# Optimization experiments

Hardware: AMD Instinct MI355X
Metric: run time of the kernel (lower is better)

The kernel has to match this reference:

```python
import jax, jax.numpy as jnp
import numpy as np

RES = (64, 64, 64)      # sim.res
INV_DX = 64.0           # sim.inv_dx (n_grid = 64)
P_MASS = 1.0            # sim.p_mass
N = 4_000_000           # n_particles


def setup_inputs() -> dict:
    key = jax.random.key(0)
    k1, k2 = jax.random.split(key)
    # positions in [0.05, 0.95)^3 so the 3x3x3 B-spline stencil stays in-grid
    x = jax.random.uniform(k1, (N, 3), jnp.float32) * 0.9 + 0.05
    x_ref = jax.random.uniform(k2, (N, 3), jnp.float32) * 0.9 + 0.05
    return {"x": x, "x_ref": x_ref}


def _density(x):
    # x: [N, 3] particle positions in [0, 1)
    xs = x * INV_DX
    base = jnp.floor(xs - 0.5).astype(jnp.int32)  # [N, 3]; positions > 0 so floor == trunc (.int() in torch)
    fx = xs - base.astype(x.dtype)                # [N, 3]
    # quadratic B-spline weights, stacked -> [3, N, 3]
    w = jnp.stack([0.5 * (1.5 - fx) ** 2,
                   0.75 - (fx - 1.0) ** 2,
                   0.5 * (fx - 0.5) ** 2])
    density = jnp.zeros(RES, x.dtype)
    # scatter-add over the 27 stencil offsets (equivalent to the unique/mask dedup sum)
    for i in range(3):
        for j in range(3):
            for k in range(3):
                weight = w[i, :, 0] * w[j, :, 1] * w[k, :, 2]  # [N]
                idx = base + jnp.array([i, j, k], jnp.int32)   # [N, 3]
                density = density.at[idx[:, 0], idx[:, 1], idx[:, 2]].add(weight * P_MASS)
    return density


def reference(x, x_ref):
    density = _density(x)
    density_ref = _density(x_ref)
    return jnp.abs(density - density_ref).sum()
```

## Files before the change

kernel.cpp:

```cpp
#include <hip/hip_runtime.h>

#define NRES 64
#define GRID_CELLS (NRES * NRES * NRES)
#define TILE_CELLS 16384
#define TPB 1024
#define QI 2
#define FILL_QUADS (TPB * QI)
#define ZBINS 64
#define NSLABS2 32
#define GC 8
#define CAP 150016u
#define MAXC 32
#define FXS 4194304.0f
#define INV_FXS (1.0f / 4194304.0f)
#define QS 2097152.0f
typedef unsigned long long u64;
typedef unsigned u32;
typedef unsigned short u16;


__device__ __forceinline__ u32 quantc(float v) {
    return (u32)(v * QS + 0.5f);
}
__device__ __forceinline__ int cell_from_q(u32 q) {
    float s = (float)q * (1.0f / 32768.0f);
    int c = (int)(s - 0.5f);
    return min(max(c, 0), 63);
}

__global__ __launch_bounds__(TPB)
void fused_fill_kernel(const float* __restrict__ x, const float* __restrict__ xr,
                       int n, u32* __restrict__ cursor, u64* __restrict__ bins) {
    __shared__ u64 stage[FILL_QUADS * 4];
    __shared__ u32 h[ZBINS];
    __shared__ u32 lb[ZBINS];
    __shared__ u32 gb[ZBINS];
    const int tid = threadIdx.x;
    if (tid < ZBINS) h[tid] = 0;
    __syncthreads();

    const int Q = n >> 2;
    const int GQ = 2 * Q;
    const int g0 = blockIdx.x * FILL_QUADS + tid;

    u64 ent[QI][4];
    u32 lsl[QI][4];
    bool val[QI];

#pragma unroll
    for (int it = 0; it < QI; ++it) {
        int g = g0 + it * TPB;
        val[it] = (g < GQ);
        if (val[it]) {
            int inx = (g < Q);
            const float* __restrict__ p = inx ? (x + 12 * (size_t)g)
                                              : (xr + 12 * (size_t)(g - Q));
            float4 a = ((const float4*)p)[0];
            float4 b = ((const float4*)p)[1];
            float4 c = ((const float4*)p)[2];
            u64 sgn = inx ? 0ull : (1ull << 63);
            float px[4] = {a.x, a.w, b.z, c.y};
            float py[4] = {a.y, b.x, b.w, c.z};
            float pz[4] = {a.z, b.y, c.x, c.w};
#pragma unroll
            for (int q = 0; q < 4; ++q) {
                u32 xq = quantc(px[q]);
                u32 yq = quantc(py[q]);
                u32 zq = quantc(pz[q]);
                ent[it][q] = (u64)xq | ((u64)yq << 21) | ((u64)zq << 42) | sgn;
                int bz = cell_from_q(zq);
                lsl[it][q] = atomicAdd(&h[bz], 1u);
            }
        }
    }
    __syncthreads();

    if (tid < 64) {
        u32 c = h[tid];
        u32 acc = c;
#pragma unroll
        for (int off = 1; off < 64; off <<= 1) {
            u32 o = __shfl_up(acc, off, 64);
            if (tid >= off) acc += o;
        }
        lb[tid] = acc - c;
        gb[tid] = c ? atomicAdd(&cursor[tid], c) : 0u;
    }
    __syncthreads();

#pragma unroll
    for (int it = 0; it < QI; ++it) {
        if (val[it]) {
#pragma unroll
            for (int q = 0; q < 4; ++q) {
                u64 v = ent[it][q];
                int bz = cell_from_q((u32)((v >> 42) & 0x1FFFFFu));
                stage[lb[bz] + lsl[it][q]] = v;
            }
        }
    }
    __syncthreads();

    const int wid = tid >> 6, lane = tid & 63;
    for (int b = wid; b < ZBINS; b += TPB / 64) {
        u32 cnt = h[b];
        u32 l0 = lb[b];
        u32 g  = gb[b];
        u64* __restrict__ dst = bins + (size_t)b * CAP;
        for (u32 i = lane; i < cnt; i += 64) {
            u32 slot = g + i;
            if (slot < CAP) dst[slot] = stage[l0 + i];
        }
    }
}

__global__ __launch_bounds__(TPB)
void bin_scatter_kernel(const u64* __restrict__ bins,
                        const u32* __restrict__ cursor,
                        int* __restrict__ partial) {
    __shared__ int tile[TILE_CELLS];
    const int slab  = blockIdx.x / GC;
    const int chunk = blockIdx.x - slab * GC;

    for (int i = threadIdx.x; i < TILE_CELLS / 4; i += TPB)
        reinterpret_cast<int4*>(tile)[i] = make_int4(0, 0, 0, 0);
    __syncthreads();

    const u32 b0 = (u32)(2 * slab), b1 = b0 + 1;
    u32 c0 = cursor[b0]; if (c0 > CAP) c0 = CAP;
    u32 c1 = cursor[b1]; if (c1 > CAP) c1 = CAP;
    u32 cnt = c0 + c1;
    u32 per = (cnt + (u32)GC - 1u) / (u32)GC;
    u32 i0 = (u32)chunk * per;
    u32 i1 = i0 + per;
    if (i1 > cnt) i1 = cnt;

    for (u32 i = i0 + threadIdx.x; i < i1; i += TPB) {
        u32 idx = (i < c0) ? (b0 * CAP + i) : (b1 * CAP + (i - c0));
        u64 v = bins[idx];
        float xs = (float)(u32)(v & 0x1FFFFFu) * (1.0f / 32768.0f);
        float ys = (float)(u32)((v >> 21) & 0x1FFFFFu) * (1.0f / 32768.0f);
        float zs = (float)(u32)((v >> 42) & 0x1FFFFFu) * (1.0f / 32768.0f);
        float fsgn = (v >> 63) ? -FXS : FXS;

        int bx = (int)(xs - 0.5f);
        int by = (int)(ys - 0.5f);
        int bz = (int)(zs - 0.5f);
        float fx = xs - (float)bx, fy = ys - (float)by, fz = zs - (float)bz;

        float wx0 = 0.5f * (1.5f - fx) * (1.5f - fx);
        float wx1 = 0.75f - (fx - 1.0f) * (fx - 1.0f);
        float wx2 = 0.5f * (fx - 0.5f) * (fx - 0.5f);
        float wy0 = 0.5f * (1.5f - fy) * (1.5f - fy);
        float wy1 = 0.75f - (fy - 1.0f) * (fy - 1.0f);
        float wy2 = 0.5f * (fy - 0.5f) * (fy - 0.5f);
        float wzv[3];
        wzv[0] = 0.5f * (1.5f - fz) * (1.5f - fz);
        wzv[1] = 0.75f - (fz - 1.0f) * (fz - 1.0f);
        wzv[2] = 0.5f * (fz - 0.5f) * (fz - 0.5f);

        float wxy[9];
        wxy[0] = wx0 * wy0; wxy[1] = wx0 * wy1; wxy[2] = wx0 * wy2;
        wxy[3] = wx1 * wy0; wxy[4] = wx1 * wy1; wxy[5] = wx1 * wy2;
        wxy[6] = wx2 * wy0; wxy[7] = wx2 * wy1; wxy[8] = wx2 * wy2;

        int basexy = bx * 64 + by;
        int zlo = bz - 2 * slab;
#pragma unroll
        for (int k = 0; k < 3; ++k) {
            float wzS = wzv[k] * fsgn;
            int a = (zlo + k) * 4096 + basexy;
#pragma unroll
            for (int i2 = 0; i2 < 3; ++i2)
#pragma unroll
                for (int j2 = 0; j2 < 3; ++j2)
                    atomicAdd(&tile[a + i2 * 64 + j2],
                              __float2int_rn(wxy[i2 * 3 + j2] * wzS));
        }
    }
    __syncthreads();

    int* __restrict__ dst = partial + (size_t)blockIdx.x * TILE_CELLS;
    for (int i = threadIdx.x; i < TILE_CELLS / 4; i += TPB)
        reinterpret_cast<int4*>(dst)[i] = reinterpret_cast<const int4*>(tile)[i];
}

__global__ void int_reduce_kernel(const int* __restrict__ partial,
                                  float* __restrict__ out) {
    int tid = blockIdx.x * blockDim.x + threadIdx.x;
    int z  = tid >> 12;
    int xy = tid & 4095;
    int s0 = z >> 1, zl0 = z & 1;
    int sum = 0;
    const int* __restrict__ p0 =
        partial + (size_t)(s0 * GC) * TILE_CELLS + zl0 * 4096 + xy;
#pragma unroll
    for (int g = 0; g < GC; ++g) sum += p0[(size_t)g * TILE_CELLS];
    if (s0 > 0) {
        const int* __restrict__ p1 =
            partial + (size_t)((s0 - 1) * GC) * TILE_CELLS + (zl0 + 2) * 4096 + xy;
#pragma unroll
        for (int g = 0; g < GC; ++g) sum += p1[(size_t)g * TILE_CELLS];
    }
    float v = fabsf((float)sum) * INV_FXS;
#pragma unroll
    for (int off = 32; off > 0; off >>= 1) v += __shfl_down(v, off, 64);
    __shared__ float wsum[4];
    int lane = threadIdx.x & 63, wid = threadIdx.x >> 6;
    if (lane == 0) wsum[wid] = v;
    __syncthreads();
    if (threadIdx.x == 0) atomicAdd(out, wsum[0] + wsum[1] + wsum[2] + wsum[3]);
}


__global__ __launch_bounds__(TPB)
void slab_scatter_kernel(const float* __restrict__ x,
                         const float* __restrict__ xr,
                         int n, int C, float* __restrict__ partial) {
    __shared__ float tile[TILE_CELLS];
    const int slab  = blockIdx.x / C;
    const int chunk = blockIdx.x - slab * C;
    const int z0 = slab * 4;

    for (int i = threadIdx.x; i < TILE_CELLS; i += TPB) tile[i] = 0.0f;
    __syncthreads();

    const int per = (n + C - 1) / C;
    const int p0 = chunk * per;
    const int p1 = min(n, p0 + per);

    for (int f = 0; f < 2; ++f) {
        const float* __restrict__ p = f ? xr : x;
        const float sgn = f ? -1.0f : 1.0f;
        for (int i = p0 + (int)threadIdx.x; i < p1; i += TPB) {
            float zs = p[3 * i + 2] * 64.0f;
            int bz = (int)floorf(zs - 0.5f);
            int zlo = bz - z0;
            if (zlo > 3 || zlo + 2 < 0) continue;

            float xs = p[3 * i + 0] * 64.0f;
            float ys = p[3 * i + 1] * 64.0f;
            int bx = (int)floorf(xs - 0.5f);
            int by = (int)floorf(ys - 0.5f);
            float fx = xs - (float)bx, fy = ys - (float)by, fz = zs - (float)bz;

            float wx0 = 0.5f * (1.5f - fx) * (1.5f - fx);
            float wx1 = 0.75f - (fx - 1.0f) * (fx - 1.0f);
            float wx2 = 0.5f * (fx - 0.5f) * (fx - 0.5f);
            float wy0 = 0.5f * (1.5f - fy) * (1.5f - fy);
            float wy1 = 0.75f - (fy - 1.0f) * (fy - 1.0f);
            float wy2 = 0.5f * (fy - 0.5f) * (fy - 0.5f);
            float wzv[3];
            wzv[0] = 0.5f * (1.5f - fz) * (1.5f - fz);
            wzv[1] = 0.75f - (fz - 1.0f) * (fz - 1.0f);
            wzv[2] = 0.5f * (fz - 0.5f) * (fz - 0.5f);

            float wxy[9];
            wxy[0] = sgn * wx0 * wy0; wxy[1] = sgn * wx0 * wy1; wxy[2] = sgn * wx0 * wy2;
            wxy[3] = sgn * wx1 * wy0; wxy[4] = sgn * wx1 * wy1; wxy[5] = sgn * wx1 * wy2;
            wxy[6] = sgn * wx2 * wy0; wxy[7] = sgn * wx2 * wy1; wxy[8] = sgn * wx2 * wy2;

            int base = (bx * 64 + by) * 4;
#pragma unroll
            for (int k = 0; k < 3; ++k) {
                int zl = zlo + k;
                if (zl < 0 || zl >= 4) continue;
                float wzk = wzv[k];
                int a = base + zl;
#pragma unroll
                for (int i2 = 0; i2 < 3; ++i2)
#pragma unroll
                    for (int j2 = 0; j2 < 3; ++j2)
                        atomicAdd(&tile[a + i2 * 256 + j2 * 4], wxy[i2 * 3 + j2] * wzk);
            }
        }
    }
    __syncthreads();

    float* __restrict__ dst = partial + (size_t)chunk * GRID_CELLS;
    for (int t = threadIdx.x; t < NRES * NRES; t += TPB) {
        float4 v = *reinterpret_cast<const float4*>(&tile[t * 4]);
        *reinterpret_cast<float4*>(&dst[t * 64 + z0]) = v;
    }
}

__global__ void reduce_kernel(const float* __restrict__ partial, int C,
                              float* __restrict__ out) {
    int cell = blockIdx.x * blockDim.x + threadIdx.x;
    float s = 0.0f;
    for (int c = 0; c < C; ++c) s += partial[(size_t)c * GRID_CELLS + cell];
    s = fabsf(s);
#pragma unroll
    for (int off = 32; off > 0; off >>= 1) s += __shfl_down(s, off, 64);
    __shared__ float wsum[4];
    int lane = threadIdx.x & 63, wid = threadIdx.x >> 6;
    if (lane == 0) wsum[wid] = s;
    __syncthreads();
    if (threadIdx.x == 0) atomicAdd(out, wsum[0] + wsum[1] + wsum[2] + wsum[3]);
}

extern "C" void kernel_launch(void* const* d_in, const int* in_sizes, int n_in,
                              void* d_out, int out_size, void* d_ws, size_t ws_size,
                              hipStream_t stream) {
    const float* x  = (const float*)d_in[0];
    const float* xr = (const float*)d_in[1];
    float* out = (float*)d_out;
    char* ws = (char*)d_ws;

    int n = in_sizes[0] / 3;

    const size_t OFF_CUR  = 0;
    const size_t OFF_BINS = 4096;
    const size_t binsBytes = (size_t)ZBINS * CAP * sizeof(u64);
    const size_t OFF_PART = OFF_BINS + binsBytes;
    const size_t partBytes = (size_t)NSLABS2 * GC * TILE_CELLS * 4;
    const size_t gridBytes = (size_t)GRID_CELLS * sizeof(float);

    hipMemsetAsync(out, 0, sizeof(float), stream);

    if ((n & 3) == 0 && (u32)(2 * n) <= ZBINS * (CAP - 10000u)
        && ws_size >= OFF_PART + partBytes) {
        u32* cursor  = (u32*)(ws + OFF_CUR);
        u64* bins    = (u64*)(ws + OFF_BINS);
        int* partial = (int*)(ws + OFF_PART);

        int GQ = (n >> 2) * 2;
        int fillBlocks = (GQ + FILL_QUADS - 1) / FILL_QUADS;

        hipMemsetAsync(cursor, 0, ZBINS * sizeof(u32), stream);
        fused_fill_kernel<<<fillBlocks, TPB, 0, stream>>>(x, xr, n, cursor, bins);
        bin_scatter_kernel<<<NSLABS2 * GC, TPB, 0, stream>>>(bins, cursor, partial);
        int_reduce_kernel<<<GRID_CELLS / 256, 256, 0, stream>>>(partial, out);
    } else {
        float* partial = (float*)ws;
        int C = (int)(ws_size / gridBytes);
        if (C > MAXC) C = MAXC;
        if (C < 1) C = 1;
        slab_scatter_kernel<<<16 * C, TPB, 0, stream>>>(x, xr, n, C, partial);
        reduce_kernel<<<GRID_CELLS / 256, 256, 0, stream>>>(partial, C, out);
    }
}
```

Baseline: 122.0 us.

## Pack adjacent cell contributions into 64-bit LDS atomics with split sign tiles

Each particle's three y-adjacent cell weights are packed into two 64-bit shared-memory atomicAdds instead of three 32-bit ones, cutting the LDS atomic count from 27 to 18 per particle. Because carries from the low word would corrupt the high word, weights are kept unsigned. Positive and negative (reference) particles now go into separate tiles, which are subtracted when written out. This doubles LDS usage to 128KB per block. That likely drops the number of resident blocks per CU and assumes per-cell sums never overflow 32 bits.

```diff
diff --git a/kernel.cpp b/kernel.cpp
--- a/kernel.cpp
+++ b/kernel.cpp
@@ -118,12 +118,13 @@
 void bin_scatter_kernel(const u64* __restrict__ bins,
                         const u32* __restrict__ cursor,
                         int* __restrict__ partial) {
-    __shared__ int tile[TILE_CELLS];
+    __shared__ u64 tileLL[TILE_CELLS];
+    int* intTile = (int*)tileLL;
     const int slab  = blockIdx.x / GC;
     const int chunk = blockIdx.x - slab * GC;
 
-    for (int i = threadIdx.x; i < TILE_CELLS / 4; i += TPB)
-        reinterpret_cast<int4*>(tile)[i] = make_int4(0, 0, 0, 0);
+    for (int i = threadIdx.x; i < TILE_CELLS * 2 / 4; i += TPB)
+        reinterpret_cast<int4*>(intTile)[i] = make_int4(0, 0, 0, 0);
     __syncthreads();
 
     const u32 b0 = (u32)(2 * slab), b1 = b0 + 1;
@@ -141,7 +142,7 @@
         float xs = (float)(u32)(v & 0x1FFFFFu) * (1.0f / 32768.0f);
         float ys = (float)(u32)((v >> 21) & 0x1FFFFFu) * (1.0f / 32768.0f);
         float zs = (float)(u32)((v >> 42) & 0x1FFFFFu) * (1.0f / 32768.0f);
-        float fsgn = (v >> 63) ? -FXS : FXS;
+        u64* __restrict__ t64 = tileLL + ((v >> 63) ? 8192 : 0);
 
         int bx = (int)(xs - 0.5f);
         int by = (int)(ys - 0.5f);
@@ -159,30 +160,41 @@
         wzv[1] = 0.75f - (fz - 1.0f) * (fz - 1.0f);
         wzv[2] = 0.5f * (fz - 0.5f) * (fz - 0.5f);
 
-        float wxy[9];
-        wxy[0] = wx0 * wy0; wxy[1] = wx0 * wy1; wxy[2] = wx0 * wy2;
-        wxy[3] = wx1 * wy0; wxy[4] = wx1 * wy1; wxy[5] = wx1 * wy2;
-        wxy[6] = wx2 * wy0; wxy[7] = wx2 * wy1; wxy[8] = wx2 * wy2;
+        float wxr[3] = {wx0, wx1, wx2};
+        float wyr[3] = {wy0, wy1, wy2};
 
         int basexy = bx * 64 + by;
         int zlo = bz - 2 * slab;
 #pragma unroll
         for (int k = 0; k < 3; ++k) {
-            float wzS = wzv[k] * fsgn;
-            int a = (zlo + k) * 4096 + basexy;
-#pragma unroll
-            for (int i2 = 0; i2 < 3; ++i2)
-#pragma unroll
-                for (int j2 = 0; j2 < 3; ++j2)
-                    atomicAdd(&tile[a + i2 * 64 + j2],
-                              __float2int_rn(wxy[i2 * 3 + j2] * wzS));
+            float wzS = wzv[k] * FXS;
+            int a0 = (zlo + k) * 4096 + basexy;
+#pragma unroll
+            for (int i2 = 0; i2 < 3; ++i2) {
+                float wxz = wxr[i2] * wzS;
+                u32 q0 = (u32)__float2int_rn(wyr[0] * wxz);
+                u32 q1 = (u32)__float2int_rn(wyr[1] * wxz);
+                u32 q2 = (u32)__float2int_rn(wyr[2] * wxz);
+                int a = a0 + i2 * 64;
+                int e = a & 1;
+                int w0 = a >> 1;
+                u64 p0 = e ? ((u64)q0 << 32) : ((u64)q0 | ((u64)q1 << 32));
+                u64 p1 = e ? ((u64)q1 | ((u64)q2 << 32)) : (u64)q2;
+                atomicAdd(&t64[w0], p0);
+                atomicAdd(&t64[w0 + 1], p1);
+            }
         }
     }
     __syncthreads();
 
     int* __restrict__ dst = partial + (size_t)blockIdx.x * TILE_CELLS;
-    for (int i = threadIdx.x; i < TILE_CELLS / 4; i += TPB)
-        reinterpret_cast<int4*>(dst)[i] = reinterpret_cast<const int4*>(tile)[i];
+    for (int i = threadIdx.x; i < TILE_CELLS / 4; i += TPB) {
+        int4 P = reinterpret_cast<const int4*>(intTile)[i];
+        int4 N = reinterpret_cast<const int4*>(intTile + TILE_CELLS)[i];
+        int4 d;
+        d.x = P.x - N.x; d.y = P.y - N.y; d.z = P.z - N.z; d.w = P.w - N.w;
+        reinterpret_cast<int4*>(dst)[i] = d;
+    }
 }
 
 __global__ void int_reduce_kernel(const int* __restrict__ partial,
```

After: 129.4 us. 6.1% more time.
